# Kernel tuning notes

Hardware: AMD Instinct MI355X
Metric: run time of the kernel (lower is better)

## Reference

```python
import jax, jax.numpy as jnp
import numpy as np

N_NODES = 100_000
N_EDGES = 1_600_000
IN_F = 256
HID = 256
OUT_F = 256
BN_EPS = 1e-5


def make_quaternion_mul(kernel):
    # kernel: [d, 4m] -> hamilton: [4d, 4m]
    dim = kernel.shape[1] // 4
    r, i, j, k = jnp.split(kernel, 4, axis=1)
    r2 = jnp.concatenate([r, -i, -j, -k], axis=0)
    i2 = jnp.concatenate([i, r, -k, j], axis=0)
    j2 = jnp.concatenate([j, k, r, -i], axis=0)
    k2 = jnp.concatenate([k, -j, i, r], axis=0)
    return jnp.concatenate([r2, i2, j2, k2], axis=1)


def setup_inputs() -> dict:
    key = jax.random.key(0)
    ks = jax.random.split(key, 6)
    x = jax.random.normal(ks[0], (N_NODES, IN_F), dtype=jnp.float32)
    rows = jax.random.randint(ks[1], (N_EDGES,), 0, N_NODES, dtype=jnp.int32)
    cols = jax.random.randint(ks[2], (N_EDGES,), 0, N_NODES, dtype=jnp.int32)
    edge_vals = jax.random.uniform(ks[3], (N_EDGES,), dtype=jnp.float32)
    stdv1 = np.sqrt(6.0 / (IN_F // 4 + HID))
    weight1 = jax.random.uniform(ks[4], (IN_F // 4, HID), dtype=jnp.float32,
                                 minval=-stdv1, maxval=stdv1)
    stdv2 = np.sqrt(6.0 / (HID // 4 + OUT_F))
    weight2 = jax.random.uniform(ks[5], (HID // 4, OUT_F), dtype=jnp.float32,
                                 minval=-stdv2, maxval=stdv2)
    gamma = jnp.ones((HID,), dtype=jnp.float32)
    beta = jnp.zeros((HID,), dtype=jnp.float32)
    return {"x": x, "rows": rows, "cols": cols, "edge_vals": edge_vals,
            "weight1": weight1, "weight2": weight2, "gamma": gamma, "beta": beta}


def reference(x, rows, cols, edge_vals, weight1, weight2, gamma, beta):
    hamilton1 = make_quaternion_mul(weight1)  # [IN_F, HID]
    hamilton2 = make_quaternion_mul(weight2)  # [HID, OUT_F]
    # spmm: new_x[r] = sum_e adj[r,c]*x[c] over edges (r=rows, c=cols)
    gathered = edge_vals[:, None] * x[cols]               # [E, IN_F]
    new_x = jax.ops.segment_sum(gathered, rows, num_segments=N_NODES)
    out1 = new_x @ hamilton1                              # [N, HID]
    # BatchNorm1d (training mode): biased batch stats over nodes
    mean = jnp.mean(out1, axis=0)
    var = jnp.mean(jnp.square(out1 - mean), axis=0)
    out1 = (out1 - mean) * jax.lax.rsqrt(var + BN_EPS) * gamma + beta
    out1 = jnp.tanh(out1)
    return out1 @ hamilton2                               # [N, OUT_F]
```

## Files before the change

kernel.cpp:

```cpp
#include <hip/hip_runtime.h>
#include <hip/hip_bf16.h>
#include <hip/hip_fp16.h>
#include <math.h>


#define FDIM 256
#define NREP 32
#define CH 2048

typedef __attribute__((ext_vector_type(8))) _Float16 f16x8;
typedef __attribute__((ext_vector_type(4))) float f32x4;

static __device__ inline ushort f2h_bits(float x) {
    _Float16 h = (_Float16)x;
    return __builtin_bit_cast(unsigned short, h);
}
static __device__ inline float h2f(ushort u) {
    return (float)__builtin_bit_cast(_Float16, u);
}
static __device__ inline float fast_tanh(float x) {
    float e = __expf(2.f * x);
    return 1.f - 2.f * __builtin_amdgcn_rcpf(e + 1.f);
}

static __device__ void build_hfrag(const float* __restrict__ w, ushort* __restrict__ hf,
                                   int t) {
    const int   comp_t[16] = {0,1,2,3,  1,0,3,2,  2,3,0,1,  3,2,1,0};
    const float sign_t[16] = {1,1,1,1, -1,1,1,-1, -1,-1,1,1, -1,1,-1,1};
    int f = t >> 6, lane = t & 63;
    int tile = f >> 3, kk = f & 7;
    int col = tile * 16 + (lane & 15);
    int b = col >> 6, q = col & 63;
    ushort o[8];
#pragma unroll
    for (int j = 0; j < 8; ++j) {
        int k = kk * 32 + ((lane >> 4) << 3) + j;
        int a = k >> 6, p = k & 63;
        int ab = a * 4 + b;
        float v = sign_t[ab] * w[p * 256 + comp_t[ab] * 64 + q];
        o[j] = f2h_bits(v);
    }
    *(ushort4*)(hf + (size_t)t * 8)     = make_ushort4(o[0], o[1], o[2], o[3]);
    *(ushort4*)(hf + (size_t)t * 8 + 4) = make_ushort4(o[4], o[5], o[6], o[7]);
}

__global__ __launch_bounds__(256) void k_initp1(const float* __restrict__ w1,
                                                const float* __restrict__ w2,
                                                ushort* __restrict__ h1f,
                                                ushort* __restrict__ h2f,
                                                float* __restrict__ statsR,
                                                const int* __restrict__ rows,
                                                int* __restrict__ CM,
                                                int E, int nchunk, int NB) {
    int b = blockIdx.x;
    if (b < 32) {
        build_hfrag(w1, h1f, b * 256 + threadIdx.x);
        return;
    }
    if (b < 64) {
        build_hfrag(w2, h2f, (b - 32) * 256 + threadIdx.x);
        return;
    }
    if (b < 80) {
        int slot = (b - 64) * 256 + threadIdx.x;
        *(float4*)(statsR + slot * 4) = make_float4(0.f, 0.f, 0.f, 0.f);
        return;
    }
    __shared__ int lc[256];
    int t = threadIdx.x, c = b - 80;
    lc[t] = 0;
    __syncthreads();
#pragma unroll
    for (int i = 0; i < 8; ++i) {
        int e = c * CH + i * 256 + t;
        if (e < E) atomicAdd(&lc[rows[e] >> 9], 1);
    }
    __syncthreads();
    if (t < NB) CM[t * nchunk + c] = lc[t];
}

__global__ __launch_bounds__(256) void k_p2(const int* __restrict__ CM,
                                            int* __restrict__ PO,
                                            int* __restrict__ BT, int nchunk) {
    __shared__ int ts[256];
    int t = threadIdx.x, b = blockIdx.x;
    int base = b * nchunk;
    int lex[4], s = 0;
#pragma unroll
    for (int i = 0; i < 4; ++i) {
        int c = t * 4 + i;
        int v = (c < nchunk) ? CM[base + c] : 0;
        lex[i] = s;
        s += v;
    }
    ts[t] = s;
    __syncthreads();
    for (int off = 1; off < 256; off <<= 1) {
        int v = (t >= off) ? ts[t - off] : 0;
        __syncthreads();
        ts[t] += v;
        __syncthreads();
    }
    int excl = ts[t] - s;
#pragma unroll
    for (int i = 0; i < 4; ++i) {
        int c = t * 4 + i;
        if (c < nchunk) PO[base + c] = excl + lex[i];
    }
    if (t == 255) BT[b] = ts[255];
}

__global__ __launch_bounds__(256) void k_p3(const int* __restrict__ rows,
                                            const int* __restrict__ cols,
                                            const float* __restrict__ vals,
                                            const int* __restrict__ PO,
                                            const int* __restrict__ BT,
                                            uint2* __restrict__ tmp2,
                                            int E, int nchunk, int NB) {
    __shared__ int sBB[256];
    __shared__ int sPO[256];
    __shared__ int sLC[256];
    int t = threadIdx.x, c = blockIdx.x;
    int own = (t < NB) ? BT[t] : 0;
    sBB[t] = own;
    sPO[t] = (t < NB) ? PO[t * nchunk + c] : 0;
    sLC[t] = 0;
    __syncthreads();
    for (int off = 1; off < 256; off <<= 1) {
        int v = (t >= off) ? sBB[t - off] : 0;
        __syncthreads();
        sBB[t] += v;
        __syncthreads();
    }
    sBB[t] -= own;
    __syncthreads();
#pragma unroll
    for (int i = 0; i < 8; ++i) {
        int e = c * CH + i * 256 + t;
        if (e < E) {
            int r = rows[e];
            int b = r >> 9;
            int rank = atomicAdd(&sLC[b], 1);
            int pos = sBB[b] + sPO[b] + rank;
            unsigned int hv = f2h_bits(vals[e]);
            tmp2[pos] = make_uint2((unsigned int)cols[e] | (hv << 17),
                                   (unsigned int)r);
        }
    }
}

__global__ __launch_bounds__(1024) void k_p4(const uint2* __restrict__ tmp2,
                                             const int* __restrict__ BT,
                                             unsigned int* __restrict__ ew,
                                             uint2* __restrict__ offs2,
                                             int N, int NB) {
    __shared__ int sBB[256];
    __shared__ int sH[512];
    __shared__ int sHp[512];
    __shared__ int sOp[512];
    __shared__ int sC[512];
    int t = threadIdx.x, b = blockIdx.x;
    int own = 0;
    if (t < 256) {
        own = (t < NB) ? BT[t] : 0;
        sBB[t] = own;
    }
    __syncthreads();
    for (int off = 1; off < 256; off <<= 1) {
        int v = (t < 256 && t >= off) ? sBB[t - off] : 0;
        __syncthreads();
        if (t < 256) sBB[t] += v;
        __syncthreads();
    }
    if (t < 256) sBB[t] -= own;
    if (t < 512) sH[t] = 0;
    __syncthreads();
    const int base = sBB[b];
    const int basePad = sBB[b] + b * 4096;
    const int nE = BT[b];
    const int rbase = b << 9;
    for (int i = t; i < nE; i += 1024)
        atomicAdd(&sH[(int)tmp2[base + i].y - rbase], 1);
    __syncthreads();
    if (t < 512) {
        int hp = (sH[t] + 7) & ~7;
        sHp[t] = hp;
        sOp[t] = hp;
    }
    __syncthreads();
    for (int off = 1; off < 512; off <<= 1) {
        int v = (t < 512 && t >= off) ? sOp[t - off] : 0;
        __syncthreads();
        if (t < 512) sOp[t] += v;
        __syncthreads();
    }
    if (t < 512) {
        sOp[t] -= sHp[t];
        int r = rbase + t;
        if (r < N) offs2[r] = make_uint2((unsigned int)(basePad + sOp[t]),
                                         (unsigned int)sHp[t]);
        sC[t] = 0;
    }
    __syncthreads();
    for (int i = t; i < nE; i += 1024) {
        uint2 u = tmp2[base + i];
        int lr = (int)u.y - rbase;
        int p = atomicAdd(&sC[lr], 1);
        ew[basePad + sOp[lr] + p] = u.x;
    }
    if (t < 512) {
        int e0 = basePad + sOp[t] + sH[t];
        int e1 = basePad + sOp[t] + sHp[t];
        for (int e = e0; e < e1; ++e) ew[e] = 0u;
    }
}

__global__ __launch_bounds__(256) void k_gemm1(const float* __restrict__ X,
                                               const ushort* __restrict__ Bf,
                                               ushort* __restrict__ Y, int N) {
    __shared__ float4 lds4[2048];
    ushort* lds = (ushort*)lds4;
    const int t = threadIdx.x;
    const int w = t >> 6, lane = t & 63;
    const int r0 = blockIdx.x * 64 + w * 16;
    const int q = (lane >> 4) & 3, l = lane & 15;
    const int kbase = q * 8;
    const int rA = min(r0 + l, N - 1);

    f16x8 af[8];
#pragma unroll
    for (int kk = 0; kk < 8; ++kk) {
        const float* p = X + (size_t)rA * 256 + kk * 32 + kbase;
        float4 v0 = *(const float4*)p;
        float4 v1 = *(const float4*)(p + 4);
        f16x8 a;
        a[0] = (_Float16)v0.x; a[1] = (_Float16)v0.y;
        a[2] = (_Float16)v0.z; a[3] = (_Float16)v0.w;
        a[4] = (_Float16)v1.x; a[5] = (_Float16)v1.y;
        a[6] = (_Float16)v1.z; a[7] = (_Float16)v1.w;
        af[kk] = a;
    }

    for (int g = 0; g < 4; ++g) {
        {
            const float4* s4 = (const float4*)(Bf + (size_t)g * 16384);
#pragma unroll
            for (int i = 0; i < 8; ++i) lds4[i * 256 + t] = s4[i * 256 + t];
        }
        __syncthreads();

        f32x4 acc[4];
#pragma unroll
        for (int tg = 0; tg < 4; ++tg) acc[tg] = (f32x4){0.f, 0.f, 0.f, 0.f};

#pragma unroll
        for (int tg = 0; tg < 4; ++tg)
#pragma unroll
            for (int kk = 0; kk < 8; ++kk) {
                f16x8 b = *(const f16x8*)(lds + ((tg * 8 + kk) * 64 + lane) * 8);
                acc[tg] = __builtin_amdgcn_mfma_f32_16x16x32_f16(af[kk], b, acc[tg], 0, 0, 0);
            }
        __syncthreads();

        {
            ushort* cw = lds + w * 1024;
#pragma unroll
            for (int tg = 0; tg < 4; ++tg)
#pragma unroll
                for (int j = 0; j < 4; ++j)
                    cw[(q * 4 + j) * 64 + tg * 16 + l] = f2h_bits(acc[tg][j]);
        }
        __syncthreads();
        {
            int gcol0 = g * 64;
#pragma unroll
            for (int p = 0; p < 2; ++p) {
                uint4 rd = *(const uint4*)(lds + w * 1024 + p * 512 + lane * 8);
                int row = r0 + p * 8 + (lane >> 3);
                int col = gcol0 + (lane & 7) * 8;
                if (row < N) *(uint4*)(Y + (size_t)row * 256 + col) = rd;
            }
        }
        __syncthreads();
    }
}

__global__ __launch_bounds__(256) void k_spmm(const ushort* __restrict__ Y,
                                              const uint2* __restrict__ offs2,
                                              const unsigned int* __restrict__ ew,
                                              ushort* __restrict__ O,
                                              float* __restrict__ statsR,
                                              int n, int W) {
    __shared__ float ls_s[4][256];
    __shared__ float ls_q[4][256];
    const int tid = threadIdx.x;
    const int w = tid >> 6, lane = tid & 63;
    const int gw = blockIdx.x * 4 + w;

    float s0 = 0.f, s1 = 0.f, s2 = 0.f, s3 = 0.f;
    float q0 = 0.f, q1 = 0.f, q2 = 0.f, q3 = 0.f;

    for (int k = 0; k < 4; ++k) {
        int row = gw + k * W;
        bool ok = row < n;
        int r = ok ? row : 0;
        uint2 bc = offs2[r];
        int cnt = ok ? (int)bc.y : 0;
        int g = cnt >> 3;
        const unsigned int* ep = ew + bc.x;

        __half2 a01 = __builtin_bit_cast(__half2, 0u);
        __half2 a23 = __builtin_bit_cast(__half2, 0u);
        unsigned int wv[8];
        if (g > 0) {
#pragma unroll
            for (int i = 0; i < 8; ++i) wv[i] = ep[i];
        }
        for (int gi = 0; gi < g; ++gi) {
            unsigned int wn[8];
            bool more = (gi + 1) < g;
            if (more) {
#pragma unroll
                for (int i = 0; i < 8; ++i) wn[i] = ep[(gi + 1) * 8 + i];
            }
#pragma unroll
            for (int i = 0; i < 8; ++i) {
                unsigned int wd = (unsigned int)__builtin_amdgcn_readfirstlane((int)wv[i]);
                unsigned int c = wd & 0x1FFFFu;
                unsigned int hv = wd >> 17;
                __half2 vv = __builtin_bit_cast(__half2, hv | (hv << 16));
                uint2 u = *(const uint2*)(Y + (size_t)c * 256 + lane * 4);
                a01 = __hfma2(__builtin_bit_cast(__half2, u.x), vv, a01);
                a23 = __hfma2(__builtin_bit_cast(__half2, u.y), vv, a23);
            }
            if (more) {
#pragma unroll
                for (int i = 0; i < 8; ++i) wv[i] = wn[i];
            }
        }
        if (ok) {
            uint2 o = make_uint2(__builtin_bit_cast(unsigned int, a01),
                                 __builtin_bit_cast(unsigned int, a23));
            *(uint2*)(O + (size_t)r * 512 + lane * 4) = o;
        }
        float2 f01 = __half22float2(a01);
        float2 f23 = __half22float2(a23);
        s0 += f01.x; q0 = fmaf(f01.x, f01.x, q0);
        s1 += f01.y; q1 = fmaf(f01.y, f01.y, q1);
        s2 += f23.x; q2 = fmaf(f23.x, f23.x, q2);
        s3 += f23.y; q3 = fmaf(f23.y, f23.y, q3);
    }

    int rep = blockIdx.x & (NREP - 1);
    *(float4*)&ls_s[w][lane * 4] = make_float4(s0, s1, s2, s3);
    *(float4*)&ls_q[w][lane * 4] = make_float4(q0, q1, q2, q3);
    __syncthreads();
    float sv = ls_s[0][tid] + ls_s[1][tid] + ls_s[2][tid] + ls_s[3][tid];
    float qv = ls_q[0][tid] + ls_q[1][tid] + ls_q[2][tid] + ls_q[3][tid];
    atomicAdd(&statsR[rep * 256 + tid], sv);
    atomicAdd(&statsR[NREP * 256 + rep * 256 + tid], qv);
}

__global__ __launch_bounds__(256) void k_gemm2(void* __restrict__ Av,
                                               const ushort* __restrict__ Bf,
                                               const float* __restrict__ statsR,
                                               const float* __restrict__ gamma,
                                               const float* __restrict__ beta, int N) {
    __shared__ float4 lds4[2048];
    ushort* lds = (ushort*)lds4;
    __shared__ float sscl[256], sshf[256];
    const int t = threadIdx.x;
    const int w = t >> 6, lane = t & 63;
    const int r0 = blockIdx.x * 64 + w * 16;
    const int q = (lane >> 4) & 3, l = lane & 15;
    const int kbase = q * 8;
    const int rA = min(r0 + l, N - 1);

    {
        float s = 0.f, qq = 0.f;
#pragma unroll
        for (int i = 0; i < NREP; ++i) {
            s += statsR[i * 256 + t];
            qq += statsR[NREP * 256 + i * 256 + t];
        }
        float invn = 1.0f / (float)N;
        float mean = s * invn;
        float var = qq * invn - mean * mean;
        float inv = rsqrtf(var + 1e-5f);
        float gg = gamma[t] * inv;
        sscl[t] = gg;
        sshf[t] = beta[t] - mean * gg;
        __syncthreads();
    }

    const ushort* X = (const ushort*)Av;
    f16x8 af[8];
#pragma unroll
    for (int kk = 0; kk < 8; ++kk) {
        const ushort* p = X + (size_t)rA * 512 + kk * 32 + kbase;
        ushort4 u0 = *(const ushort4*)p;
        ushort4 u1 = *(const ushort4*)(p + 4);
        float4 s0 = *(const float4*)&sscl[kk * 32 + kbase];
        float4 s1 = *(const float4*)&sscl[kk * 32 + kbase + 4];
        float4 h0 = *(const float4*)&sshf[kk * 32 + kbase];
        float4 h1 = *(const float4*)&sshf[kk * 32 + kbase + 4];
        f16x8 a;
        a[0] = (_Float16)fast_tanh(fmaf(h2f(u0.x), s0.x, h0.x));
        a[1] = (_Float16)fast_tanh(fmaf(h2f(u0.y), s0.y, h0.y));
        a[2] = (_Float16)fast_tanh(fmaf(h2f(u0.z), s0.z, h0.z));
        a[3] = (_Float16)fast_tanh(fmaf(h2f(u0.w), s0.w, h0.w));
        a[4] = (_Float16)fast_tanh(fmaf(h2f(u1.x), s1.x, h1.x));
        a[5] = (_Float16)fast_tanh(fmaf(h2f(u1.y), s1.y, h1.y));
        a[6] = (_Float16)fast_tanh(fmaf(h2f(u1.z), s1.z, h1.z));
        a[7] = (_Float16)fast_tanh(fmaf(h2f(u1.w), s1.w, h1.w));
        af[kk] = a;
    }

    float* Cf = (float*)Av;
    for (int g = 0; g < 4; ++g) {
        {
            const float4* s4 = (const float4*)(Bf + (size_t)g * 16384);
#pragma unroll
            for (int i = 0; i < 8; ++i) lds4[i * 256 + t] = s4[i * 256 + t];
        }
        __syncthreads();

        f32x4 acc[4];
#pragma unroll
        for (int tg = 0; tg < 4; ++tg) acc[tg] = (f32x4){0.f, 0.f, 0.f, 0.f};

#pragma unroll
        for (int tg = 0; tg < 4; ++tg)
#pragma unroll
            for (int kk = 0; kk < 8; ++kk) {
                f16x8 b = *(const f16x8*)(lds + ((tg * 8 + kk) * 64 + lane) * 8);
                acc[tg] = __builtin_amdgcn_mfma_f32_16x16x32_f16(af[kk], b, acc[tg], 0, 0, 0);
            }
        __syncthreads();

        {
            float* cw = (float*)lds4 + w * 1024;
#pragma unroll
            for (int tg = 0; tg < 4; ++tg)
#pragma unroll
                for (int j = 0; j < 4; ++j)
                    cw[(q * 4 + j) * 64 + tg * 16 + l] = acc[tg][j];
        }
        __syncthreads();
        {
            int gcol0 = g * 64;
#pragma unroll
            for (int p = 0; p < 4; ++p) {
                f32x4 rd = *(const f32x4*)((float*)lds4 + w * 1024 + p * 256 + lane * 4);
                int row = r0 + p * 4 + (lane >> 4);
                int col = gcol0 + (lane & 15) * 4;
                if (row < N)
                    __builtin_nontemporal_store(rd, (f32x4*)(Cf + (size_t)row * 256 + col));
            }
        }
        __syncthreads();
    }
}

extern "C" void kernel_launch(void* const* d_in, const int* in_sizes, int n_in,
                              void* d_out, int out_size, void* d_ws, size_t ws_size,
                              hipStream_t stream) {
    const float* x     = (const float*)d_in[0];
    const int* rows    = (const int*)d_in[1];
    const int* cols    = (const int*)d_in[2];
    const float* evin  = (const float*)d_in[3];
    const float* w1    = (const float*)d_in[4];
    const float* w2    = (const float*)d_in[5];
    const float* gamma = (const float*)d_in[6];
    const float* beta  = (const float*)d_in[7];
    float* out = (float*)d_out;

    const int N = in_sizes[0] / FDIM;
    const int E = in_sizes[1];
    const int NB = (N + 511) >> 9;
    const int nchunk = (E + CH - 1) / CH;

    char* ws = (char*)d_ws;
    size_t o = 0;
    auto alloc = [&](size_t bytes) -> char* {
        char* p = ws + o;
        o += (bytes + 255) & ~(size_t)255;
        return p;
    };
    ushort* h1f  = (ushort*)alloc(128 * 64 * 8 * 2);
    ushort* h2f  = (ushort*)alloc(128 * 64 * 8 * 2);
    ushort* y    = (ushort*)alloc((size_t)N * 256 * 2);
    float* statsR = (float*)alloc(2 * NREP * 256 * 4);
    int*   CM    = (int*)alloc((size_t)NB * nchunk * 4);
    int*   PO    = (int*)alloc((size_t)NB * nchunk * 4);
    int*   BT    = (int*)alloc(256 * 4);
    uint2* tmp2  = (uint2*)alloc((size_t)E * 8);
    unsigned int* ewp = (unsigned int*)alloc(((size_t)E + (size_t)NB * 4096 + 16) * 4);
    uint2* offs2 = (uint2*)alloc((size_t)N * 8);

    k_initp1<<<80 + nchunk, 256, 0, stream>>>(w1, w2, h1f, h2f, statsR,
                                              rows, CM, E, nchunk, NB);
    k_p2<<<NB, 256, 0, stream>>>(CM, PO, BT, nchunk);
    k_p3<<<nchunk, 256, 0, stream>>>(rows, cols, evin, PO, BT, tmp2, E, nchunk, NB);
    k_p4<<<NB, 1024, 0, stream>>>(tmp2, BT, ewp, offs2, N, NB);

    int gblk = (N + 63) / 64;
    k_gemm1<<<gblk, 256, 0, stream>>>(x, h1f, y, N);
    int W = (N + 3) / 4;
    int sblk = (W + 3) / 4;
    k_spmm<<<sblk, 256, 0, stream>>>(y, offs2, ewp, (ushort*)out, statsR, N, W);
    k_gemm2<<<gblk, 256, 0, stream>>>(out, h2f, statsR, gamma, beta, N);
}
```

Baseline: 246.6 us.

## Split SpMM feature dimension in halves and group rows contiguously per block

The SpMM kernel now processes each row in two feature halves, with separate blocks handling 128 columns each. Each lane accumulates a single half2 instead of two, and rows are assigned contiguously (16 per block group) instead of strided by W. This doubles the number of waves for more latency hiding and keeps the 8 blocks that share rows adjacent in launch order, aiming for better L2 reuse of edge lists. The cost is that every edge list and index is read twice, and each gather is a narrower 4-byte access per lane.

New measurement: 241.7 us. 1.02x faster.

```diff
diff --git a/kernel.cpp b/kernel.cpp
--- a/kernel.cpp
+++ b/kernel.cpp
@@ -289,19 +289,21 @@
                                               const uint2* __restrict__ offs2,
                                               const unsigned int* __restrict__ ew,
                                               ushort* __restrict__ O,
-                                              float* __restrict__ statsR,
-                                              int n, int W) {
-    __shared__ float ls_s[4][256];
-    __shared__ float ls_q[4][256];
+                                              float* __restrict__ statsR, int n) {
+    __shared__ float ls_s[4][128];
+    __shared__ float ls_q[4][128];
     const int tid = threadIdx.x;
     const int w = tid >> 6, lane = tid & 63;
-    const int gw = blockIdx.x * 4 + w;
-
-    float s0 = 0.f, s1 = 0.f, s2 = 0.f, s3 = 0.f;
-    float q0 = 0.f, q1 = 0.f, q2 = 0.f, q3 = 0.f;
+    const int slot = blockIdx.x & 7;
+    const int rbg  = blockIdx.x >> 3;
+    const int half = slot >> 2;
+    const int rb   = rbg * 4 + (slot & 3);
+    const int fb   = half * 128 + lane * 2;
+
+    float s0 = 0.f, s1 = 0.f, q0 = 0.f, q1 = 0.f;
 
     for (int k = 0; k < 4; ++k) {
-        int row = gw + k * W;
+        int row = rb * 16 + w * 4 + k;
         bool ok = row < n;
         int r = ok ? row : 0;
         uint2 bc = offs2[r];
@@ -309,8 +311,7 @@
         int g = cnt >> 3;
         const unsigned int* ep = ew + bc.x;
 
-        __half2 a01 = __builtin_bit_cast(__half2, 0u);
-        __half2 a23 = __builtin_bit_cast(__half2, 0u);
+        __half2 acc = __builtin_bit_cast(__half2, 0u);
         unsigned int wv[8];
         if (g > 0) {
 #pragma unroll
@@ -329,9 +330,8 @@
                 unsigned int c = wd & 0x1FFFFu;
                 unsigned int hv = wd >> 17;
                 __half2 vv = __builtin_bit_cast(__half2, hv | (hv << 16));
-                uint2 u = *(const uint2*)(Y + (size_t)c * 256 + lane * 4);
-                a01 = __hfma2(__builtin_bit_cast(__half2, u.x), vv, a01);
-                a23 = __hfma2(__builtin_bit_cast(__half2, u.y), vv, a23);
+                unsigned int u = *(const unsigned int*)(Y + (size_t)c * 256 + fb);
+                acc = __hfma2(__builtin_bit_cast(__half2, u), vv, acc);
             }
             if (more) {
 #pragma unroll
@@ -339,26 +339,24 @@
             }
         }
         if (ok) {
-            uint2 o = make_uint2(__builtin_bit_cast(unsigned int, a01),
-                                 __builtin_bit_cast(unsigned int, a23));
-            *(uint2*)(O + (size_t)r * 512 + lane * 4) = o;
-        }
-        float2 f01 = __half22float2(a01);
-        float2 f23 = __half22float2(a23);
+            *(unsigned int*)(O + (size_t)r * 512 + fb) =
+                __builtin_bit_cast(unsigned int, acc);
+        }
+        float2 f01 = __half22float2(acc);
         s0 += f01.x; q0 = fmaf(f01.x, f01.x, q0);
         s1 += f01.y; q1 = fmaf(f01.y, f01.y, q1);
-        s2 += f23.x; q2 = fmaf(f23.x, f23.x, q2);
-        s3 += f23.y; q3 = fmaf(f23.y, f23.y, q3);
-    }
-
-    int rep = blockIdx.x & (NREP - 1);
-    *(float4*)&ls_s[w][lane * 4] = make_float4(s0, s1, s2, s3);
-    *(float4*)&ls_q[w][lane * 4] = make_float4(q0, q1, q2, q3);
-    __syncthreads();
-    float sv = ls_s[0][tid] + ls_s[1][tid] + ls_s[2][tid] + ls_s[3][tid];
-    float qv = ls_q[0][tid] + ls_q[1][tid] + ls_q[2][tid] + ls_q[3][tid];
-    atomicAdd(&statsR[rep * 256 + tid], sv);
-    atomicAdd(&statsR[NREP * 256 + rep * 256 + tid], qv);
+    }
+
+    int rep = rbg & (NREP - 1);
+    *(float2*)&ls_s[w][lane * 2] = make_float2(s0, s1);
+    *(float2*)&ls_q[w][lane * 2] = make_float2(q0, q1);
+    __syncthreads();
+    if (tid < 128) {
+        float sv = ls_s[0][tid] + ls_s[1][tid] + ls_s[2][tid] + ls_s[3][tid];
+        float qv = ls_q[0][tid] + ls_q[1][tid] + ls_q[2][tid] + ls_q[3][tid];
+        atomicAdd(&statsR[rep * 256 + half * 128 + tid], sv);
+        atomicAdd(&statsR[NREP * 256 + rep * 256 + half * 128 + tid], qv);
+    }
 }
 
 __global__ __launch_bounds__(256) void k_gemm2(void* __restrict__ Av,
@@ -506,8 +504,8 @@
 
     int gblk = (N + 63) / 64;
     k_gemm1<<<gblk, 256, 0, stream>>>(x, h1f, y, N);
-    int W = (N + 3) / 4;
-    int sblk = (W + 3) / 4;
-    k_spmm<<<sblk, 256, 0, stream>>>(y, offs2, ewp, (ushort*)out, statsR, N, W);
+    int nRB = (N + 15) / 16;
+    int nRBG = (nRB + 3) / 4;
+    k_spmm<<<nRBG * 8, 256, 0, stream>>>(y, offs2, ewp, (ushort*)out, statsR, N);
     k_gemm2<<<gblk, 256, 0, stream>>>(out, h2f, statsR, gamma, beta, N);
 }
```
